# Optimization experiments

Hardware: AMD Instinct MI355X
Metric: run time of the kernel (lower is better)

## Reference

```python
import jax, jax.numpy as jnp
import numpy as np

D_EMBED = 1024
N_HEAD = 16
LEN_TRIM = 1024
LN_EPS = 1e-5


def setup_inputs() -> dict:
    key = jax.random.key(0)
    ks = jax.random.split(key, 8)
    B = 2
    h_q = jax.random.normal(ks[0], (B, LEN_TRIM, D_EMBED), jnp.float32)
    h_kv1 = jax.random.normal(ks[1], (B, LEN_TRIM, D_EMBED), jnp.float32)
    h_kv2 = jax.random.normal(ks[2], (B, 2 * LEN_TRIM, D_EMBED), jnp.float32)
    mask = jax.random.uniform(ks[3], (B, LEN_TRIM, 1), jnp.float32)
    in_proj_w = jax.random.normal(ks[4], (3 * D_EMBED, D_EMBED), jnp.float32) * 0.02
    in_proj_b = jnp.zeros((3 * D_EMBED,), jnp.float32)
    out_w = jax.random.normal(ks[5], (D_EMBED, D_EMBED), jnp.float32) * 0.02
    out_b = jnp.zeros((D_EMBED,), jnp.float32)
    ln_g = jnp.ones((D_EMBED,), jnp.float32)
    ln_b = jnp.zeros((D_EMBED,), jnp.float32)
    return dict(h_q=h_q, h_kv1=h_kv1, h_kv2=h_kv2, mask=mask,
                in_proj_w=in_proj_w, in_proj_b=in_proj_b,
                out_w=out_w, out_b=out_b, ln_g=ln_g, ln_b=ln_b)


def _layernorm(x, g, b):
    mu = jnp.mean(x, axis=-1, keepdims=True)
    var = jnp.mean(jnp.square(x - mu), axis=-1, keepdims=True)
    return (x - mu) * jax.lax.rsqrt(var + LN_EPS) * g + b


def reference(h_q, h_kv1, h_kv2, mask, in_proj_w, in_proj_b, out_w, out_b, ln_g, ln_b):
    B, L, D = h_q.shape
    H = N_HEAD
    dh = D // H
    h_kv = jnp.concatenate((h_kv1, h_kv2), axis=1)  # (B, 3L, D)
    S = h_kv.shape[1]
    Wq, Wk, Wv = jnp.split(in_proj_w, 3, axis=0)
    bq, bk, bv = jnp.split(in_proj_b, 3, axis=0)
    q = (h_q @ Wq.T + bq).reshape(B, L, H, dh).transpose(0, 2, 1, 3)   # (B,H,L,dh)
    k = (h_kv @ Wk.T + bk).reshape(B, S, H, dh).transpose(0, 2, 1, 3)  # (B,H,S,dh)
    v = (h_kv @ Wv.T + bv).reshape(B, S, H, dh).transpose(0, 2, 1, 3)
    scores = jnp.einsum('bhld,bhsd->bhls', q, k) / jnp.sqrt(jnp.float32(dh))
    block = jnp.triu(jnp.ones((L, L), bool), k=1)
    mask_causal = jnp.concatenate((block, block, block), axis=-1)  # (L, S)
    scores = jnp.where(mask_causal, -jnp.inf, scores)
    attn = jax.nn.softmax(scores, axis=-1)
    ctx = jnp.einsum('bhls,bhsd->bhld', attn, v).transpose(0, 2, 1, 3).reshape(B, L, D)
    attn_out = ctx @ out_w.T + out_b
    return _layernorm(h_q + attn_out, ln_g, ln_b) * mask
```

## Files before the change

kernel.cpp:

```cpp
#include <hip/hip_runtime.h>
#include <stdint.h>

typedef unsigned short u16;
typedef unsigned int u32;
typedef __bf16 bf16x8 __attribute__((ext_vector_type(8)));
typedef float floatx4 __attribute__((ext_vector_type(4)));
typedef u16 u16x8 __attribute__((ext_vector_type(8)));

__device__ __forceinline__ u16 f2bf(float f) {
    __bf16 h = (__bf16)f;
    return __builtin_bit_cast(u16, h);
}

__device__ __forceinline__ void gll16(const u16* g, u16* l) {
    typedef __attribute__((address_space(1))) u32 gu32;
    typedef __attribute__((address_space(3))) u32 lu32;
    __builtin_amdgcn_global_load_lds((gu32*)g, (lu32*)l, 16, 0, 0);
}

__global__ __launch_bounds__(256) void cvt_all(const float* __restrict__ hq,
                                               const float* __restrict__ kv1,
                                               const float* __restrict__ kv2,
                                               const float* __restrict__ win,
                                               u16* __restrict__ a_q,
                                               u16* __restrict__ a_kv,
                                               u16* __restrict__ wb) {
    const int NQ = 262144, NKV = 786432, NW = 393216;
    int i = blockIdx.x * 256 + threadIdx.x;
    const int stride = gridDim.x * 256;
    for (; i < NQ + NKV + NW; i += stride) {
        const float* src; u16* dst;
        if (i < NQ) {
            src = hq + (long long)i * 8; dst = a_q + (long long)i * 8;
        } else if (i < NQ + NKV) {
            int c = i - NQ;
            int row = c >> 7;
            int col = (c & 127) * 8;
            int b = row >= 3072, r = row - b * 3072;
            src = (r < 1024) ? kv1 + ((long long)(b * 1024 + r)) * 1024 + col
                             : kv2 + ((long long)(b * 2048 + (r - 1024))) * 1024 + col;
            dst = a_kv + (long long)row * 1024 + col;
        } else {
            int c = i - (NQ + NKV);
            src = win + (long long)c * 8; dst = wb + (long long)c * 8;
        }
        floatx4 x = *(const floatx4*)src;
        floatx4 y = *(const floatx4*)(src + 4);
        u16x8 o;
        #pragma unroll
        for (int j = 0; j < 4; j++) { o[j] = f2bf(x[j]); o[4 + j] = f2bf(y[j]); }
        *(u16x8*)dst = o;
    }
}

__global__ __launch_bounds__(256) void cvt_bf16(const float* __restrict__ in,
                                                u16* __restrict__ out, int n8) {
    int i = blockIdx.x * 256 + threadIdx.x;
    const int stride = gridDim.x * 256;
    for (; i < n8; i += stride) {
        floatx4 a = *(const floatx4*)(in + (long long)i * 8);
        floatx4 b = *(const floatx4*)(in + (long long)i * 8 + 4);
        u16x8 o;
        #pragma unroll
        for (int j = 0; j < 4; j++) { o[j] = f2bf(a[j]); o[4 + j] = f2bf(b[j]); }
        *(u16x8*)(out + (long long)i * 8) = o;
    }
}

__global__ __launch_bounds__(256) void gemm_proj(const u16* __restrict__ aq,
                                                 const u16* __restrict__ akv,
                                                 const u16* __restrict__ wb,
                                                 const float* __restrict__ bias,
                                                 u16* __restrict__ Qo,
                                                 u16* __restrict__ Ko,
                                                 u16* __restrict__ Vo) {
    __shared__ u16 lds[2][2][8192];
    const int tid = threadIdx.x;
    const int wave = tid >> 6, lane = tid & 63;
    const int lane16 = lane & 15, quad = lane >> 4;
    const int bid = blockIdx.x;
    const int g = (bid & 7) * 112 + (bid >> 3);
    const bool qblk = g < 128;
    int my, nx;
    if (qblk) { my = g >> 3; nx = g & 7; }
    else { int gg = g - 128; my = gg >> 4; nx = gg & 15; }
    const int rowBase = my * 128;
    const int colBase = nx * 128;
    const int wrow = (qblk ? 0 : 1024) + colBase;
    const int wm = (wave >> 1) * 64, wn = (wave & 1) * 64;

    floatx4 acc[4][4];
    #pragma unroll
    for (int am = 0; am < 4; am++)
        #pragma unroll
        for (int bn = 0; bn < 4; bn++) acc[am][bn] = floatx4{0.f, 0.f, 0.f, 0.f};

    const int srow8 = tid >> 3;
    const int scol = ((tid & 7) ^ (srow8 & 7)) * 8;
    const u16* aS = (qblk ? aq : akv) + (long long)(rowBase + srow8) * 1024 + scol;
    const u16* bS = wb + (long long)(wrow + srow8) * 1024 + scol;
    u16* lbase = &lds[0][0][0];
    const int ldst = wave * 512;

    const int cko0 = ((quad ^ (lane16 & 7)) * 8);
    const int cko1 = (((4 + quad) ^ (lane16 & 7)) * 8);

    {
        u16* dA = lbase; u16* dB = lbase + 8192;
        #pragma unroll
        for (int j = 0; j < 4; j++) {
            gll16(aS + j * 32768, dA + j * 2048 + ldst);
            gll16(bS + j * 32768, dB + j * 2048 + ldst);
        }
    }
    __syncthreads();

    int buf = 0;
    for (int t = 0; t < 16; t++) {
        if (t < 15) {
            const int k0 = (t + 1) * 64;
            u16* dA = lbase + (buf ^ 1) * 16384;
            u16* dB = dA + 8192;
            #pragma unroll
            for (int j = 0; j < 4; j++) {
                gll16(aS + j * 32768 + k0, dA + j * 2048 + ldst);
                gll16(bS + j * 32768 + k0, dB + j * 2048 + ldst);
            }
        }
        const u16* Ab = lbase + buf * 16384;
        const u16* Bb = Ab + 8192;
        u16x8 a0[4], a1[4], b0[4], b1[4];
        #pragma unroll
        for (int i = 0; i < 4; i++) {
            a0[i] = *(const u16x8*)&Ab[(wm + i * 16 + lane16) * 64 + cko0];
            a1[i] = *(const u16x8*)&Ab[(wm + i * 16 + lane16) * 64 + cko1];
            b0[i] = *(const u16x8*)&Bb[(wn + i * 16 + lane16) * 64 + cko0];
            b1[i] = *(const u16x8*)&Bb[(wn + i * 16 + lane16) * 64 + cko1];
        }
        #pragma unroll
        for (int am = 0; am < 4; am++)
            #pragma unroll
            for (int bn = 0; bn < 4; bn++)
                acc[am][bn] = __builtin_amdgcn_mfma_f32_16x16x32_bf16(
                    __builtin_bit_cast(bf16x8, a0[am]),
                    __builtin_bit_cast(bf16x8, b0[bn]), acc[am][bn], 0, 0, 0);
        #pragma unroll
        for (int am = 0; am < 4; am++)
            #pragma unroll
            for (int bn = 0; bn < 4; bn++)
                acc[am][bn] = __builtin_amdgcn_mfma_f32_16x16x32_bf16(
                    __builtin_bit_cast(bf16x8, a1[am]),
                    __builtin_bit_cast(bf16x8, b1[bn]), acc[am][bn], 0, 0, 0);
        __syncthreads();
        buf ^= 1;
    }

    const float* bcol = bias + (qblk ? 0 : 1024) + colBase;
    u16* Cb; int colLoc;
    if (qblk)        { Cb = Qo; colLoc = colBase; }
    else if (nx < 8) { Cb = Ko; colLoc = colBase; }
    else             { Cb = Vo; colLoc = colBase - 1024; }
    #pragma unroll
    for (int am = 0; am < 4; am++)
        #pragma unroll
        for (int bn = 0; bn < 4; bn++)
            #pragma unroll
            for (int r = 0; r < 4; r++) {
                int row = rowBase + wm + am * 16 + quad * 4 + r;
                int col = wn + bn * 16 + lane16;
                float v = acc[am][bn][r] + bcol[col];
                Cb[(long long)row * 1024 + colLoc + col] = f2bf(v);
            }
}

__global__ __launch_bounds__(256) void gemm_out(const u16* __restrict__ ctx,
                                                const u16* __restrict__ wob,
                                                const float* __restrict__ bias,
                                                float* __restrict__ ao0,
                                                float* __restrict__ ao1) {
    __shared__ u16 lds[2][2][8192];
    const int tid = threadIdx.x;
    const int wave = tid >> 6, lane = tid & 63;
    const int lane16 = lane & 15, quad = lane >> 4;
    const int bid = blockIdx.x;
    const int g = (bid & 7) * 32 + (bid >> 3);
    const int my = g >> 4;
    const int nx = (g & 15) >> 1;
    const int kh = g & 1;
    const int rowBase = my * 128, colBase = nx * 128, kbase = kh * 512;
    const int wm = (wave >> 1) * 64, wn = (wave & 1) * 64;

    floatx4 acc[4][4];
    #pragma unroll
    for (int am = 0; am < 4; am++)
        #pragma unroll
        for (int bn = 0; bn < 4; bn++) acc[am][bn] = floatx4{0.f, 0.f, 0.f, 0.f};

    const int srow8 = tid >> 3;
    const int scol = ((tid & 7) ^ (srow8 & 7)) * 8;
    const u16* aS = ctx + (long long)(rowBase + srow8) * 1024 + kbase + scol;
    const u16* bS = wob + (long long)(colBase + srow8) * 1024 + kbase + scol;
    u16* lbase = &lds[0][0][0];
    const int ldst = wave * 512;
    const int cko0 = ((quad ^ (lane16 & 7)) * 8);
    const int cko1 = (((4 + quad) ^ (lane16 & 7)) * 8);

    {
        u16* dA = lbase; u16* dB = lbase + 8192;
        #pragma unroll
        for (int j = 0; j < 4; j++) {
            gll16(aS + j * 32768, dA + j * 2048 + ldst);
            gll16(bS + j * 32768, dB + j * 2048 + ldst);
        }
    }
    __syncthreads();

    int buf = 0;
    for (int t = 0; t < 8; t++) {
        if (t < 7) {
            const int k0 = (t + 1) * 64;
            u16* dA = lbase + (buf ^ 1) * 16384;
            u16* dB = dA + 8192;
            #pragma unroll
            for (int j = 0; j < 4; j++) {
                gll16(aS + j * 32768 + k0, dA + j * 2048 + ldst);
                gll16(bS + j * 32768 + k0, dB + j * 2048 + ldst);
            }
        }
        const u16* Ab = lbase + buf * 16384;
        const u16* Bb = Ab + 8192;
        u16x8 a0[4], a1[4], b0[4], b1[4];
        #pragma unroll
        for (int i = 0; i < 4; i++) {
            a0[i] = *(const u16x8*)&Ab[(wm + i * 16 + lane16) * 64 + cko0];
            a1[i] = *(const u16x8*)&Ab[(wm + i * 16 + lane16) * 64 + cko1];
            b0[i] = *(const u16x8*)&Bb[(wn + i * 16 + lane16) * 64 + cko0];
            b1[i] = *(const u16x8*)&Bb[(wn + i * 16 + lane16) * 64 + cko1];
        }
        #pragma unroll
        for (int am = 0; am < 4; am++)
            #pragma unroll
            for (int bn = 0; bn < 4; bn++)
                acc[am][bn] = __builtin_amdgcn_mfma_f32_16x16x32_bf16(
                    __builtin_bit_cast(bf16x8, a0[am]),
                    __builtin_bit_cast(bf16x8, b0[bn]), acc[am][bn], 0, 0, 0);
        #pragma unroll
        for (int am = 0; am < 4; am++)
            #pragma unroll
            for (int bn = 0; bn < 4; bn++)
                acc[am][bn] = __builtin_amdgcn_mfma_f32_16x16x32_bf16(
                    __builtin_bit_cast(bf16x8, a1[am]),
                    __builtin_bit_cast(bf16x8, b1[bn]), acc[am][bn], 0, 0, 0);
        __syncthreads();
        buf ^= 1;
    }

    float* Co = kh ? ao1 : ao0;
    #pragma unroll
    for (int am = 0; am < 4; am++)
        #pragma unroll
        for (int bn = 0; bn < 4; bn++)
            #pragma unroll
            for (int r = 0; r < 4; r++) {
                int row = rowBase + wm + am * 16 + quad * 4 + r;
                int col = colBase + wn + bn * 16 + lane16;
                float v = acc[am][bn][r] + (kh == 0 ? bias[col] : 0.f);
                Co[(long long)row * 1024 + col] = v;
            }
}

__global__ __launch_bounds__(256) void attn_seg(const u16* __restrict__ Q,
                                                const u16* __restrict__ Kb,
                                                const u16* __restrict__ Vb,
                                                float* __restrict__ pO_lo,
                                                float* __restrict__ pO_hi,
                                                float* __restrict__ pml) {
    __shared__ u16 Vt[2][64 * 80];
    __shared__ u16 Ps[4][16 * 80];
    const int tid = threadIdx.x;
    const int wave = tid >> 6, lane = tid & 63;
    const int lane16 = lane & 15, quad = lane >> 4;
    const int idx_ = blockIdx.x;
    const int qhat = idx_ & 15;
    const int h   = (idx_ >> 4) & 15;
    const int b   = (idx_ >> 8) & 1;
    const int seg = idx_ >> 9;
    const int qt = b ? (15 - qhat) : qhat;
    const int l0 = qt * 64;
    const int wq = wave * 16;
    const float scale = 0.125f;

    bf16x8 qf[2];
    {
        const u16* qrow = Q + ((long long)(b * 1024 + l0 + wq + lane16)) * 1024 + h * 64;
        qf[0] = __builtin_bit_cast(bf16x8, *(const u16x8*)(qrow + quad * 8));
        qf[1] = __builtin_bit_cast(bf16x8, *(const u16x8*)(qrow + 32 + quad * 8));
    }

    const int skey = tid >> 2, sdb = (tid & 3) * 16;
    const long long bh = ((long long)b * 3072) * 1024 + h * 64;

    u16x8 kr[8], vr0, vr1;
    {
        long long o = bh + ((long long)(seg * 1024)) * 1024;
        vr0 = *(const u16x8*)(Vb + o + (long long)skey * 1024 + sdb);
        vr1 = *(const u16x8*)(Vb + o + (long long)skey * 1024 + sdb + 8);
        #pragma unroll
        for (int c = 0; c < 2; c++)
            #pragma unroll
            for (int mi = 0; mi < 4; mi++)
                kr[c * 4 + mi] = *(const u16x8*)(Kb + o + (long long)(mi * 16 + lane16) * 1024 + c * 32 + quad * 8);
    }
    #pragma unroll
    for (int i = 0; i < 8; i++) {
        Vt[0][(sdb + i) * 80 + skey]     = vr0[i];
        Vt[0][(sdb + 8 + i) * 80 + skey] = vr1[i];
    }
    __syncthreads();

    float m_i = -1e30f, l_i = 0.f;
    floatx4 o_acc[4];
    #pragma unroll
    for (int mi = 0; mi < 4; mi++) o_acc[mi] = floatx4{0.f, 0.f, 0.f, 0.f};

    for (int t = 0; t <= qt; t++) {
        const int cur = t & 1;
        const bool haveNext = t < qt;

        u16x8 nkr[8], nvr0, nvr1;
        if (haveNext) {
            long long o = bh + ((long long)(seg * 1024 + (t + 1) * 64)) * 1024;
            nvr0 = *(const u16x8*)(Vb + o + (long long)skey * 1024 + sdb);
            nvr1 = *(const u16x8*)(Vb + o + (long long)skey * 1024 + sdb + 8);
            #pragma unroll
            for (int c = 0; c < 2; c++)
                #pragma unroll
                for (int mi = 0; mi < 4; mi++)
                    nkr[c * 4 + mi] = *(const u16x8*)(Kb + o + (long long)(mi * 16 + lane16) * 1024 + c * 32 + quad * 8);
        }

        floatx4 sacc[4];
        #pragma unroll
        for (int mi = 0; mi < 4; mi++) sacc[mi] = floatx4{0.f, 0.f, 0.f, 0.f};
        #pragma unroll
        for (int c = 0; c < 2; c++)
            #pragma unroll
            for (int mi = 0; mi < 4; mi++)
                sacc[mi] = __builtin_amdgcn_mfma_f32_16x16x32_bf16(
                    __builtin_bit_cast(bf16x8, kr[c * 4 + mi]), qf[c], sacc[mi], 0, 0, 0);

        const bool diag = (t == qt);
        const int qloc = wq + lane16;
        float tmax = -1e30f;
        #pragma unroll
        for (int mi = 0; mi < 4; mi++)
            #pragma unroll
            for (int r = 0; r < 4; r++) {
                float s = sacc[mi][r] * scale;
                if (diag && (mi * 16 + quad * 4 + r) > qloc) s = -1e30f;
                sacc[mi][r] = s;
                tmax = fmaxf(tmax, s);
            }
        tmax = fmaxf(tmax, __shfl_xor(tmax, 16));
        tmax = fmaxf(tmax, __shfl_xor(tmax, 32));
        float m_new = fmaxf(m_i, tmax);
        float alpha = __expf(m_i - m_new);
        float psum = 0.f;
        #pragma unroll
        for (int mi = 0; mi < 4; mi++)
            #pragma unroll
            for (int r = 0; r < 4; r++) {
                float p = __expf(sacc[mi][r] - m_new);
                psum += p;
                Ps[wave][lane16 * 80 + mi * 16 + quad * 4 + r] = f2bf(p);
            }
        psum += __shfl_xor(psum, 16);
        psum += __shfl_xor(psum, 32);
        m_i = m_new;
        l_i = l_i * alpha + psum;
        #pragma unroll
        for (int mi = 0; mi < 4; mi++)
            #pragma unroll
            for (int r = 0; r < 4; r++) o_acc[mi][r] *= alpha;

        __builtin_amdgcn_wave_barrier();

        #pragma unroll
        for (int c = 0; c < 2; c++) {
            bf16x8 pf = __builtin_bit_cast(bf16x8,
                *(const u16x8*)&Ps[wave][lane16 * 80 + c * 32 + quad * 8]);
            #pragma unroll
            for (int mi = 0; mi < 4; mi++) {
                bf16x8 vf = __builtin_bit_cast(bf16x8,
                    *(const u16x8*)&Vt[cur][(mi * 16 + lane16) * 80 + c * 32 + quad * 8]);
                o_acc[mi] = __builtin_amdgcn_mfma_f32_16x16x32_bf16(vf, pf, o_acc[mi], 0, 0, 0);
            }
        }

        if (haveNext) {
            #pragma unroll
            for (int i = 0; i < 8; i++) {
                Vt[cur ^ 1][(sdb + i) * 80 + skey]     = nvr0[i];
                Vt[cur ^ 1][(sdb + 8 + i) * 80 + skey] = nvr1[i];
            }
            #pragma unroll
            for (int i = 0; i < 8; i++) kr[i] = nkr[i];
            __syncthreads();
        }
    }

    const int p = ((b * 16 + h) * 16 + qt) * 3 + seg;
    float* op = (p < 512) ? (pO_lo + (long long)p * 4096)
                          : (pO_hi + (long long)(p - 512) * 4096);
    if (quad == 0) {
        pml[(long long)p * 128 + (wq + lane16) * 2]     = m_i;
        pml[(long long)p * 128 + (wq + lane16) * 2 + 1] = l_i;
    }
    float* orow = op + (long long)(wq + lane16) * 64;
    #pragma unroll
    for (int mi = 0; mi < 4; mi++)
        *(floatx4*)(orow + mi * 16 + quad * 4) = o_acc[mi];
}

__global__ __launch_bounds__(256) void attn_combine(const float* __restrict__ pO_lo,
                                                    const float* __restrict__ pO_hi,
                                                    const float* __restrict__ pml,
                                                    u16* __restrict__ Ctx) {
    const int g = blockIdx.x;
    const int qt = g & 15;
    const int h  = (g >> 4) & 15;
    const int b  = g >> 8;
    const int t  = threadIdx.x;
    const int q  = t >> 2;
    const int d0 = (t & 3) * 16;
    const int p0 = g * 3;

    float m[3], l[3];
    #pragma unroll
    for (int s = 0; s < 3; s++) {
        m[s] = pml[(long long)(p0 + s) * 128 + q * 2];
        l[s] = pml[(long long)(p0 + s) * 128 + q * 2 + 1];
    }
    float M = fmaxf(m[0], fmaxf(m[1], m[2]));
    float w[3];
    #pragma unroll
    for (int s = 0; s < 3; s++) w[s] = __expf(m[s] - M);
    float L = w[0] * l[0] + w[1] * l[1] + w[2] * l[2];
    float invL = 1.0f / L;

    const float* O[3];
    #pragma unroll
    for (int s = 0; s < 3; s++) {
        int pp = p0 + s;
        O[s] = ((pp < 512) ? (pO_lo + (long long)pp * 4096)
                           : (pO_hi + (long long)(pp - 512) * 4096))
               + (long long)q * 64 + d0;
    }

    long long crow = ((long long)(b * 1024 + qt * 64 + q)) * 1024 + h * 64 + d0;
    #pragma unroll
    for (int i = 0; i < 16; i += 4) {
        floatx4 a  = *(const floatx4*)(O[0] + i);
        floatx4 bb = *(const floatx4*)(O[1] + i);
        floatx4 cc = *(const floatx4*)(O[2] + i);
        #pragma unroll
        for (int j = 0; j < 4; j++)
            Ctx[crow + i + j] = f2bf((w[0] * a[j] + w[1] * bb[j] + w[2] * cc[j]) * invL);
    }
}

__global__ __launch_bounds__(256) void ln_kernel(const float* __restrict__ AO0,
                                                 const float* __restrict__ AO1,
                                                 const float* __restrict__ HQ,
                                                 const float* __restrict__ g,
                                                 const float* __restrict__ bb,
                                                 const float* __restrict__ mask,
                                                 float* __restrict__ Out) {
    const int row = blockIdx.x;
    const int t = threadIdx.x;
    const int base = row * 1024 + t * 4;
    floatx4 a0 = *(const floatx4*)&AO0[base];
    floatx4 a1 = *(const floatx4*)&AO1[base];
    floatx4 hq = *(const floatx4*)&HQ[base];
    float x[4];
    #pragma unroll
    for (int i = 0; i < 4; i++) x[i] = a0[i] + a1[i] + hq[i];
    float s = x[0] + x[1] + x[2] + x[3];
    float ss = x[0]*x[0] + x[1]*x[1] + x[2]*x[2] + x[3]*x[3];
    #pragma unroll
    for (int off = 32; off >= 1; off >>= 1) { s += __shfl_xor(s, off); ss += __shfl_xor(ss, off); }
    __shared__ float smem[8];
    int wave = t >> 6, lane = t & 63;
    if (lane == 0) { smem[wave] = s; smem[4 + wave] = ss; }
    __syncthreads();
    s  = smem[0] + smem[1] + smem[2] + smem[3];
    ss = smem[4] + smem[5] + smem[6] + smem[7];
    float mu  = s * (1.f / 1024.f);
    float var = ss * (1.f / 1024.f) - mu * mu;
    float rs  = rsqrtf(var + 1e-5f);
    float mv  = mask[row];
    floatx4 g4 = *(const floatx4*)&g[t * 4];
    floatx4 b4 = *(const floatx4*)&bb[t * 4];
    floatx4 y4;
    #pragma unroll
    for (int i = 0; i < 4; i++) y4[i] = ((x[i] - mu) * rs * g4[i] + b4[i]) * mv;
    *(floatx4*)&Out[base] = y4;
}

extern "C" void kernel_launch(void* const* d_in, const int* in_sizes, int n_in,
                              void* d_out, int out_size, void* d_ws, size_t ws_size,
                              hipStream_t stream) {
    (void)in_sizes; (void)n_in; (void)out_size; (void)ws_size;
    const float* h_q   = (const float*)d_in[0];
    const float* h_kv1 = (const float*)d_in[1];
    const float* h_kv2 = (const float*)d_in[2];
    const float* maskp = (const float*)d_in[3];
    const float* win   = (const float*)d_in[4];
    const float* binp  = (const float*)d_in[5];
    const float* wout  = (const float*)d_in[6];
    const float* bout  = (const float*)d_in[7];
    const float* ln_g  = (const float*)d_in[8];
    const float* ln_b  = (const float*)d_in[9];
    float* outp = (float*)d_out;

    char* ws = (char*)d_ws;
    const size_t MB = 1024 * 1024;
    u16*   q_b   = (u16*)(ws);
    u16*   k_b   = (u16*)(ws + 4 * MB);
    u16*   v_b   = (u16*)(ws + 16 * MB);
    u16*   ctx_b = q_b;
    u16*   a_q   = (u16*)(ws + 28 * MB);
    u16*   a_kv  = (u16*)(ws + 32 * MB);
    u16*   wb    = (u16*)d_out;
    float* pO_lo = (float*)d_out;
    float* pO_hi = (float*)(ws + 28 * MB);
    u16*   wob   = (u16*)(ws + 28 * MB);
    float* pml   = (float*)(ws + 44 * MB);
    float* ao0   = (float*)(ws + 4 * MB);
    float* ao1   = (float*)(ws + 12 * MB);

    cvt_all<<<2048, 256, 0, stream>>>(h_q, h_kv1, h_kv2, win, a_q, a_kv, wb);
    gemm_proj<<<896, 256, 0, stream>>>(a_q, a_kv, wb, binp, q_b, k_b, v_b);
    attn_seg<<<1536, 256, 0, stream>>>(q_b, k_b, v_b, pO_lo, pO_hi, pml);
    attn_combine<<<512, 256, 0, stream>>>(pO_lo, pO_hi, pml, ctx_b);
    cvt_bf16<<<512, 256, 0, stream>>>(wout, wob, 131072);
    gemm_out<<<256, 256, 0, stream>>>(ctx_b, wob, bout, ao0, ao1);
    ln_kernel<<<2048, 256, 0, stream>>>(ao0, ao1, h_q, ln_g, ln_b, maskp, outp);
}
```

Before: 241.6 us.

## Write V transposed from projection GEMM and stream K/V tiles via direct LDS loads

```diff
diff --git a/kernel.cpp b/kernel.cpp
--- a/kernel.cpp
+++ b/kernel.cpp
@@ -6,6 +6,7 @@
 typedef __bf16 bf16x8 __attribute__((ext_vector_type(8)));
 typedef float floatx4 __attribute__((ext_vector_type(4)));
 typedef u16 u16x8 __attribute__((ext_vector_type(8)));
+typedef u16 u16x4 __attribute__((ext_vector_type(4)));
 
 __device__ __forceinline__ u16 f2bf(float f) {
     __bf16 h = (__bf16)f;
@@ -73,7 +74,7 @@
                                                  const float* __restrict__ bias,
                                                  u16* __restrict__ Qo,
                                                  u16* __restrict__ Ko,
-                                                 u16* __restrict__ Vo) {
+                                                 u16* __restrict__ VTg) {
     __shared__ u16 lds[2][2][8192];
     const int tid = threadIdx.x;
     const int wave = tid >> 6, lane = tid & 63;
@@ -156,21 +157,35 @@
     }
 
     const float* bcol = bias + (qblk ? 0 : 1024) + colBase;
-    u16* Cb; int colLoc;
-    if (qblk)        { Cb = Qo; colLoc = colBase; }
-    else if (nx < 8) { Cb = Ko; colLoc = colBase; }
-    else             { Cb = Vo; colLoc = colBase - 1024; }
-    #pragma unroll
-    for (int am = 0; am < 4; am++)
-        #pragma unroll
-        for (int bn = 0; bn < 4; bn++)
-            #pragma unroll
-            for (int r = 0; r < 4; r++) {
-                int row = rowBase + wm + am * 16 + quad * 4 + r;
+    if (qblk || nx < 8) {
+        u16* Cb = qblk ? Qo : Ko;
+        #pragma unroll
+        for (int am = 0; am < 4; am++)
+            #pragma unroll
+            for (int bn = 0; bn < 4; bn++)
+                #pragma unroll
+                for (int r = 0; r < 4; r++) {
+                    int row = rowBase + wm + am * 16 + quad * 4 + r;
+                    int col = wn + bn * 16 + lane16;
+                    float v = acc[am][bn][r] + bcol[col];
+                    Cb[(long long)row * 1024 + colBase + col] = f2bf(v);
+                }
+    } else {
+        const int b_ = rowBase >= 3072;
+        const int keyBase = rowBase - b_ * 3072 + wm;
+        #pragma unroll
+        for (int am = 0; am < 4; am++)
+            #pragma unroll
+            for (int bn = 0; bn < 4; bn++) {
                 int col = wn + bn * 16 + lane16;
-                float v = acc[am][bn][r] + bcol[col];
-                Cb[(long long)row * 1024 + colLoc + col] = f2bf(v);
-            }
+                int d = colBase - 1024 + col;
+                int key0 = keyBase + am * 16 + quad * 4;
+                u16x4 pk;
+                #pragma unroll
+                for (int r = 0; r < 4; r++) pk[r] = f2bf(acc[am][bn][r] + bcol[col]);
+                *(u16x4*)&VTg[((long long)(b_ * 1024 + d)) * 3072 + key0] = pk;
+            }
+    }
 }
 
 __global__ __launch_bounds__(256) void gemm_out(const u16* __restrict__ ctx,
@@ -271,16 +286,18 @@
 
 __global__ __launch_bounds__(256) void attn_seg(const u16* __restrict__ Q,
                                                 const u16* __restrict__ Kb,
-                                                const u16* __restrict__ Vb,
+                                                const u16* __restrict__ VTg,
                                                 float* __restrict__ pO_lo,
                                                 float* __restrict__ pO_hi,
                                                 float* __restrict__ pml) {
-    __shared__ u16 Vt[2][64 * 80];
-    __shared__ u16 Ps[4][16 * 80];
+    __shared__ u16 Kt[2][4096];
+    __shared__ u16 Vt[2][4096];
+    __shared__ u16 Ps[4][1280];
     const int tid = threadIdx.x;
     const int wave = tid >> 6, lane = tid & 63;
     const int lane16 = lane & 15, quad = lane >> 4;
-    const int idx_ = blockIdx.x;
+    const int bid = blockIdx.x;
+    const int idx_ = (bid & 7) * 192 + (bid >> 3);
     const int qhat = idx_ & 15;
     const int h   = (idx_ >> 4) & 15;
     const int b   = (idx_ >> 8) & 1;
@@ -297,26 +314,26 @@
         qf[1] = __builtin_bit_cast(bf16x8, *(const u16x8*)(qrow + 32 + quad * 8));
     }
 
-    const int skey = tid >> 2, sdb = (tid & 3) * 16;
+    const int srow = tid >> 3;
+    const int csw8 = ((tid & 7) ^ (srow & 7)) * 8;
     const long long bh = ((long long)b * 3072) * 1024 + h * 64;
-
-    u16x8 kr[8], vr0, vr1;
+    const u16* kS = Kb + bh + ((long long)(seg * 1024)) * 1024
+                    + (long long)srow * 1024 + csw8;
+    const u16* vS = VTg + ((long long)(b * 1024 + h * 64 + srow)) * 3072
+                    + seg * 1024 + csw8;
+    const int ldst = wave * 512;
+
     {
-        long long o = bh + ((long long)(seg * 1024)) * 1024;
-        vr0 = *(const u16x8*)(Vb + o + (long long)skey * 1024 + sdb);
-        vr1 = *(const u16x8*)(Vb + o + (long long)skey * 1024 + sdb + 8);
-        #pragma unroll
-        for (int c = 0; c < 2; c++)
-            #pragma unroll
-            for (int mi = 0; mi < 4; mi++)
-                kr[c * 4 + mi] = *(const u16x8*)(Kb + o + (long long)(mi * 16 + lane16) * 1024 + c * 32 + quad * 8);
-    }
-    #pragma unroll
-    for (int i = 0; i < 8; i++) {
-        Vt[0][(sdb + i) * 80 + skey]     = vr0[i];
-        Vt[0][(sdb + 8 + i) * 80 + skey] = vr1[i];
+        #pragma unroll
+        for (int j = 0; j < 2; j++) {
+            gll16(kS + j * 32768, &Kt[0][j * 2048 + ldst]);
+            gll16(vS + (long long)j * 32 * 3072, &Vt[0][j * 2048 + ldst]);
+        }
     }
     __syncthreads();
+
+    const int slot0 = ((quad ^ (lane16 & 7)) * 8);
+    const int slot1 = (((4 + quad) ^ (lane16 & 7)) * 8);
 
     float m_i = -1e30f, l_i = 0.f;
     floatx4 o_acc[4];
@@ -327,27 +344,31 @@
         const int cur = t & 1;
         const bool haveNext = t < qt;
 
-        u16x8 nkr[8], nvr0, nvr1;
         if (haveNext) {
-            long long o = bh + ((long long)(seg * 1024 + (t + 1) * 64)) * 1024;
-            nvr0 = *(const u16x8*)(Vb + o + (long long)skey * 1024 + sdb);
-            nvr1 = *(const u16x8*)(Vb + o + (long long)skey * 1024 + sdb + 8);
-            #pragma unroll
-            for (int c = 0; c < 2; c++)
-                #pragma unroll
-                for (int mi = 0; mi < 4; mi++)
-                    nkr[c * 4 + mi] = *(const u16x8*)(Kb + o + (long long)(mi * 16 + lane16) * 1024 + c * 32 + quad * 8);
+            const long long ko = (long long)(t + 1) * 65536;
+            const long long vo = (long long)(t + 1) * 64;
+            #pragma unroll
+            for (int j = 0; j < 2; j++) {
+                gll16(kS + ko + j * 32768, &Kt[cur ^ 1][j * 2048 + ldst]);
+                gll16(vS + vo + (long long)j * 32 * 3072, &Vt[cur ^ 1][j * 2048 + ldst]);
+            }
         }
 
         floatx4 sacc[4];
         #pragma unroll
         for (int mi = 0; mi < 4; mi++) sacc[mi] = floatx4{0.f, 0.f, 0.f, 0.f};
         #pragma unroll
-        for (int c = 0; c < 2; c++)
-            #pragma unroll
-            for (int mi = 0; mi < 4; mi++)
-                sacc[mi] = __builtin_amdgcn_mfma_f32_16x16x32_bf16(
-                    __builtin_bit_cast(bf16x8, kr[c * 4 + mi]), qf[c], sacc[mi], 0, 0, 0);
+        for (int mi = 0; mi < 4; mi++) {
+            u16x8 kf = *(const u16x8*)&Kt[cur][(mi * 16 + lane16) * 64 + slot0];
+            sacc[mi] = __builtin_amdgcn_mfma_f32_16x16x32_bf16(
+                __builtin_bit_cast(bf16x8, kf), qf[0], sacc[mi], 0, 0, 0);
+        }
+        #pragma unroll
+        for (int mi = 0; mi < 4; mi++) {
+            u16x8 kf = *(const u16x8*)&Kt[cur][(mi * 16 + lane16) * 64 + slot1];
+            sacc[mi] = __builtin_amdgcn_mfma_f32_16x16x32_bf16(
+                __builtin_bit_cast(bf16x8, kf), qf[1], sacc[mi], 0, 0, 0);
+        }
 
         const bool diag = (t == qt);
         const int qloc = wq + lane16;
@@ -367,13 +388,16 @@
         float alpha = __expf(m_i - m_new);
         float psum = 0.f;
         #pragma unroll
-        for (int mi = 0; mi < 4; mi++)
+        for (int mi = 0; mi < 4; mi++) {
+            u16x4 pk;
             #pragma unroll
             for (int r = 0; r < 4; r++) {
                 float p = __expf(sacc[mi][r] - m_new);
                 psum += p;
-                Ps[wave][lane16 * 80 + mi * 16 + quad * 4 + r] = f2bf(p);
-            }
+                pk[r] = f2bf(p);
+            }
+            *(u16x4*)&Ps[wave][lane16 * 80 + mi * 16 + quad * 4] = pk;
+        }
         psum += __shfl_xor(psum, 16);
         psum += __shfl_xor(psum, 32);
         m_i = m_new;
@@ -389,24 +413,16 @@
         for (int c = 0; c < 2; c++) {
             bf16x8 pf = __builtin_bit_cast(bf16x8,
                 *(const u16x8*)&Ps[wave][lane16 * 80 + c * 32 + quad * 8]);
+            const int slot = c ? slot1 : slot0;
             #pragma unroll
             for (int mi = 0; mi < 4; mi++) {
                 bf16x8 vf = __builtin_bit_cast(bf16x8,
-                    *(const u16x8*)&Vt[cur][(mi * 16 + lane16) * 80 + c * 32 + quad * 8]);
+                    *(const u16x8*)&Vt[cur][(mi * 16 + lane16) * 64 + slot]);
                 o_acc[mi] = __builtin_amdgcn_mfma_f32_16x16x32_bf16(vf, pf, o_acc[mi], 0, 0, 0);
             }
         }
 
-        if (haveNext) {
-            #pragma unroll
-            for (int i = 0; i < 8; i++) {
-                Vt[cur ^ 1][(sdb + i) * 80 + skey]     = nvr0[i];
-                Vt[cur ^ 1][(sdb + 8 + i) * 80 + skey] = nvr1[i];
-            }
-            #pragma unroll
-            for (int i = 0; i < 8; i++) kr[i] = nkr[i];
-            __syncthreads();
-        }
+        if (haveNext) __syncthreads();
     }
 
     const int p = ((b * 16 + h) * 16 + qt) * 3 + seg;
@@ -527,7 +543,7 @@
     const size_t MB = 1024 * 1024;
     u16*   q_b   = (u16*)(ws);
     u16*   k_b   = (u16*)(ws + 4 * MB);
-    u16*   v_b   = (u16*)(ws + 16 * MB);
+    u16*   vT    = (u16*)(ws + 16 * MB);
     u16*   ctx_b = q_b;
     u16*   a_q   = (u16*)(ws + 28 * MB);
     u16*   a_kv  = (u16*)(ws + 32 * MB);
@@ -540,8 +556,8 @@
     float* ao1   = (float*)(ws + 12 * MB);
 
     cvt_all<<<2048, 256, 0, stream>>>(h_q, h_kv1, h_kv2, win, a_q, a_kv, wb);
-    gemm_proj<<<896, 256, 0, stream>>>(a_q, a_kv, wb, binp, q_b, k_b, v_b);
-    attn_seg<<<1536, 256, 0, stream>>>(q_b, k_b, v_b, pO_lo, pO_hi, pml);
+    gemm_proj<<<896, 256, 0, stream>>>(a_q, a_kv, wb, binp, q_b, k_b, vT);
+    attn_seg<<<1536, 256, 0, stream>>>(q_b, k_b, vT, pO_lo, pO_hi, pml);
     attn_combine<<<512, 256, 0, stream>>>(pO_lo, pO_hi, pml, ctx_b);
     cvt_bf16<<<512, 256, 0, stream>>>(wout, wob, 131072);
     gemm_out<<<256, 256, 0, stream>>>(ctx_b, wob, bout, ao0, ao1);
```

After: 225.8 us. 6.6% less time.
